# Performance work log

Measured on AMD Instinct MI355X. Metric: run time of the kernel, lower is better.

## Reference

```python
import jax, jax.numpy as jnp
import numpy as np

N_FEAT = 32
P = 3            # patch_size
K = 4            # top-k
DS = (3, 5, 7)   # displacement windows for (l3, l2, l1)
T = 3            # n_frames
EPS = 1e-12      # F.normalize eps


def _unfold(x, ksz):
    # F.unfold(x, ksz, padding=ksz//2, stride=1): [b,c,h,w] -> [b,c,ksz*ksz,h,w]
    b, c, h, w = x.shape
    pad = ksz // 2
    xp = jnp.pad(x, ((0, 0), (0, 0), (pad, pad), (pad, pad)))
    pats = [xp[:, :, i:i + h, j:j + w] for i in range(ksz) for j in range(ksz)]
    return jnp.stack(pats, axis=2)


def _agg_unit(feat_t, feat_tm1, d, agg_w, agg_b, wp_w, wp_b):
    b, c, h, w = feat_t.shape
    p2 = P * P
    ft_u = _unfold(feat_t, P).reshape(b, c * p2, h, w)        # [b,cp2,h,w]
    ftm_u = _unfold(feat_tm1, P).reshape(b, c * p2, h, w)     # [b,cp2,h,w]
    disp = jnp.transpose(_unfold(ftm_u, d), (0, 1, 3, 4, 2))  # [b,cp2,h,w,d2]
    # cosine similarity over channel*patch dim
    ft_n = ft_u / jnp.maximum(jnp.linalg.norm(ft_u, axis=1, keepdims=True), EPS)
    disp_norm = jnp.maximum(jnp.linalg.norm(disp, axis=1), EPS)          # [b,h,w,d2]
    sim = jnp.einsum('bchw,bchwd->bhwd', ft_n, disp) / disp_norm          # [b,h,w,d2]
    _, idx = jax.lax.top_k(sim, K)                                        # [b,h,w,K]
    gath = jnp.take_along_axis(disp, idx[:, None], axis=-1)               # [b,cp2,h,w,K]
    g = gath.reshape(b, c, p2, h, w, K)
    # aggregator: Conv2d(K,1,1) == weighted sum over K + scalar bias
    aggd = jnp.einsum('bcphwk,k->bcphw', g, agg_w) + agg_b                # [b,c,p2,h,w]
    aggd = jnp.transpose(aggd, (0, 1, 3, 4, 2))                           # [b,c,h,w,p2]
    # w_proj: Conv2d(2c, c*p2, 1)
    wm = jnp.einsum('oi,bihw->bohw', wp_w, jnp.concatenate([feat_t, feat_tm1], axis=1))
    wm = wm + wp_b[None, :, None, None]
    wm = jnp.transpose(wm.reshape(b, c, p2, h, w), (0, 1, 3, 4, 2))       # [b,c,h,w,p2]
    return jnp.sum(aggd * wm, axis=-1)                                    # [b,c,h,w]


def _up2(x):
    # bilinear x2, align_corners=False (half-pixel == jax.image 'linear')
    b, c, h, w = x.shape
    return jax.image.resize(x, (b, c, 2 * h, 2 * w), method='linear')


def _pixel_shuffle(x, r):
    b, c, h, w = x.shape
    co = c // (r * r)
    x = x.reshape(b, co, r, r, h, w)
    return jnp.transpose(x, (0, 1, 4, 2, 5, 3)).reshape(b, co, h * r, w * r)


def setup_inputs() -> dict:
    key = jax.random.key(0)
    ks = jax.random.split(key, 20)
    B, C, H = 1, N_FEAT, 48
    p2 = P * P
    d = {}
    d['feats_l1'] = jax.random.normal(ks[0], (B, C, T, H, H), jnp.float32)
    d['feats_l2'] = jax.random.normal(ks[1], (B, C, T, H // 2, H // 2), jnp.float32)
    d['feats_l3'] = jax.random.normal(ks[2], (B, C, T, H // 4, H // 4), jnp.float32)
    for i, name in enumerate(['l3', 'l2', 'l1']):
        d['agg_' + name + '_w'] = jax.random.normal(ks[3 + 4 * i], (K,), jnp.float32) * 0.1
        d['agg_' + name + '_b'] = jax.random.normal(ks[4 + 4 * i], (), jnp.float32) * 0.1
        d['wp_' + name + '_w'] = jax.random.normal(ks[5 + 4 * i], (C * p2, 2 * C), jnp.float32) * 0.05
        d['wp_' + name + '_b'] = jnp.zeros((C * p2,), jnp.float32)
    d['up_w'] = jax.random.normal(ks[16], (4 * C, C * T), jnp.float32) * 0.05
    d['up_b'] = jnp.zeros((4 * C,), jnp.float32)
    return d


def reference(feats_l1, feats_l2, feats_l3,
              agg_l3_w, agg_l3_b, wp_l3_w, wp_l3_b,
              agg_l2_w, agg_l2_b, wp_l2_w, wp_l2_b,
              agg_l1_w, agg_l1_b, wp_l1_w, wp_l1_b,
              up_w, up_b):
    center = T // 2
    c1 = feats_l1[:, :, center]
    c2 = feats_l2[:, :, center]
    c3 = feats_l3[:, :, center]
    a3 = [_up2(_agg_unit(c3, feats_l3[:, :, t], DS[0], agg_l3_w, agg_l3_b, wp_l3_w, wp_l3_b))
          for t in range(T)]
    a2 = [_up2(_agg_unit(c2 + a3[t], feats_l2[:, :, t] + a3[t], DS[1], agg_l2_w, agg_l2_b, wp_l2_w, wp_l2_b))
          for t in range(T)]
    a1 = [_agg_unit(c1 + a2[t], feats_l1[:, :, t] + a2[t], DS[2], agg_l1_w, agg_l1_b, wp_l1_w, wp_l1_b)
          for t in range(T)]
    x = jnp.concatenate(a1, axis=1)                                       # [b, c*T, h, w]
    x = jnp.einsum('oi,bihw->bohw', up_w, x) + up_b[None, :, None, None]  # [b, 4c, h, w]
    return _pixel_shuffle(x, 2)                                           # [b, c, 2h, 2w]
```

## Files before the change

### kernel.cpp

```cpp
#include <hip/hip_runtime.h>
#include <math.h>


template<int D, int TS, int H, int W, bool HA>
__global__ __launch_bounds__(256, 4)
void agg_tile(const float* __restrict__ feats,
              const float* __restrict__ add,
              const float* __restrict__ agg_w,
              const float* __restrict__ agg_b,
              const float* __restrict__ wp_w,
              const float* __restrict__ wp_b,
              float* __restrict__ out)
{
    constexpr int PD = D / 2;
    constexpr int M  = PD + 1;
    constexpr int R  = TS + 2 * M;
    constexpr int S  = TS + 2;
    constexpr int S2 = S * S;
    constexpr int D2 = D * D;
    constexpr int NP = TS * TS;
    constexpr int NX = S2 * D2;
    constexpr int NSIM = NP * D2;
    constexpr int CS = 36;
    constexpr int USZ = (NP * 288 > NX + NSIM) ? NP * 288 : NX + NSIM;
    constexpr int TPW = W / TS;
    constexpr int NPA = R * R;
    constexpr int GA  = 256 / NPA;
    constexpr int NPS = S * S;
    constexpr int GS  = 256 / NPS;

    __shared__ float sA[NPA * CS];
    __shared__ float sC[NPS * CS];
    __shared__ float t2[NPA];
    __shared__ float s2[NPS];
    __shared__ float U[USZ];
    __shared__ int   sIdx[NP * 4];

    float* Xarr = U;
    float* sSim = U + NX;

    const int tid  = threadIdx.x;
    const int tile = blockIdx.x;
    const int t    = blockIdx.y;
    const int y0 = (tile / TPW) * TS;
    const int x0 = (tile % TPW) * TS;

    const float* addT = HA ? (add + (size_t)t * 32 * H * W) : nullptr;

    if (tid < NPA * GA) {
        const int pos = tid % NPA;
        const int cb  = tid / NPA;
        const int ry = pos / R, rx = pos % R;
        const int yy = y0 - M + ry, xx = x0 - M + rx;
        float* dst = sA + pos * CS;
        if (yy >= 0 && yy < H && xx >= 0 && xx < W) {
            const float* sF = feats + (((size_t)cb * 3 + t) * H + yy) * W + xx;
            const float* sD = HA ? (addT + ((size_t)cb * H + yy) * W + xx) : nullptr;
            #pragma unroll 1
            for (int c = cb; c < 32; c += GA) {
                float v = *sF; sF += GA * 3 * H * W;
                if (HA) { v += *sD; sD += GA * H * W; }
                dst[c] = v;
            }
        } else {
            #pragma unroll 1
            for (int c = cb; c < 32; c += GA) dst[c] = 0.f;
        }
    }
    if (tid < NPS * GS) {
        const int pos = tid % NPS;
        const int cb  = tid / NPS;
        const int ry = pos / S, rx = pos % S;
        const int yy = y0 - 1 + ry, xx = x0 - 1 + rx;
        float* dst = sC + pos * CS;
        if (yy >= 0 && yy < H && xx >= 0 && xx < W) {
            const float* sF = feats + (((size_t)cb * 3 + 1) * H + yy) * W + xx;
            const float* sD = HA ? (addT + ((size_t)cb * H + yy) * W + xx) : nullptr;
            #pragma unroll 1
            for (int c = cb; c < 32; c += GS) {
                float v = *sF; sF += GS * 3 * H * W;
                if (HA) { v += *sD; sD += GS * H * W; }
                dst[c] = v;
            }
        } else {
            #pragma unroll 1
            for (int c = cb; c < 32; c += GS) dst[c] = 0.f;
        }
    }
    __syncthreads();

    if (tid < S2 * D) {
        const int u  = tid / D;
        const int di = tid - u * D;
        const int uy = u / S, ux = u - uy * S;
        float4 cv[8];
        const float4* c4 = (const float4*)(sC + u * CS);
        #pragma unroll
        for (int i = 0; i < 8; ++i) cv[i] = c4[i];
        const float* arow = sA + ((uy + di) * R + ux) * CS;
        float* xrow = Xarr + u * D2 + di * D;
        #pragma unroll
        for (int dj = 0; dj < D; ++dj) {
            const float4* a4 = (const float4*)(arow + dj * CS);
            float s = 0.f;
            #pragma unroll
            for (int i = 0; i < 8; ++i) {
                float4 av = a4[i];
                s += cv[i].x * av.x + cv[i].y * av.y + cv[i].z * av.z + cv[i].w * av.w;
            }
            xrow[dj] = s;
        }
    }
    for (int e = tid; e < NPA; e += 256) {
        const float4* a4 = (const float4*)(sA + e * CS);
        float s = 0.f;
        #pragma unroll
        for (int cc = 0; cc < 8; ++cc) {
            float4 v = a4[cc];
            s += v.x * v.x + v.y * v.y + v.z * v.z + v.w * v.w;
        }
        t2[e] = s;
    }
    for (int e = tid; e < NPS; e += 256) {
        const float4* c4 = (const float4*)(sC + e * CS);
        float s = 0.f;
        #pragma unroll
        for (int cc = 0; cc < 8; ++cc) {
            float4 v = c4[cc];
            s += v.x * v.x + v.y * v.y + v.z * v.z + v.w * v.w;
        }
        s2[e] = s;
    }
    __syncthreads();

    for (int e = tid; e < NSIM; e += 256) {
        int p = e / D2, dd = e - p * D2;
        int py = p / TS, px = p - py * TS;
        int di = dd / D, dj = dd - di * D;
        int Yc = y0 + py + di - PD, Xc = x0 + px + dj - PD;
        float sim = 0.f;
        if (Yc >= 0 && Yc < H && Xc >= 0 && Xc < W) {
            float dot = 0.f, n2 = 0.f, nf = 0.f;
            #pragma unroll
            for (int qi = 0; qi < 3; ++qi)
            #pragma unroll
            for (int qj = 0; qj < 3; ++qj) {
                dot += Xarr[((py + qi) * S + (px + qj)) * D2 + dd];
                n2  += t2[(py + qi + di) * R + (px + qj + dj)];
                nf  += s2[(py + qi) * S + (px + qj)];
            }
            sim = dot / fmaxf(sqrtf(nf), 1e-12f) / fmaxf(sqrtf(n2), 1e-12f);
        }
        sSim[e] = sim;
    }
    __syncthreads();

    if (tid < NP) {
        float v0 = -3.0e38f, v1 = -3.0e38f, v2 = -3.0e38f, v3 = -3.0e38f;
        int   i0 = 0, i1 = 0, i2 = 0, i3 = 0;
        const float* row = sSim + tid * D2;
        for (int dd = 0; dd < D2; ++dd) {
            float v = row[dd];
            if (v > v0)      { v3=v2;i3=i2; v2=v1;i2=i1; v1=v0;i1=i0; v0=v;i0=dd; }
            else if (v > v1) { v3=v2;i3=i2; v2=v1;i2=i1; v1=v;i1=dd; }
            else if (v > v2) { v3=v2;i3=i2; v2=v;i2=dd; }
            else if (v > v3) { v3=v;i3=dd; }
        }
        int py = tid / TS, px = tid - (tid / TS) * TS;
        int ids[4] = {i0, i1, i2, i3};
        #pragma unroll
        for (int k = 0; k < 4; ++k) {
            int dd = ids[k];
            int di = dd / D, dj = dd - di * D;
            int Yc = y0 + py + di - PD, Xc = x0 + px + dj - PD;
            sIdx[tid * 4 + k] = (Yc >= 0 && Yc < H && Xc >= 0 && Xc < W)
                              ? (di * R + dj) * CS : -1;
        }
    }
    __syncthreads();

    const float4* wp4 = (const float4*)wp_w;
    for (int o = tid; o < 288; o += 256) {
        float4 w[8];
        #pragma unroll
        for (int i = 0; i < 8; ++i) w[i] = wp4[o * 16 + i];
        const float wb = wp_b[o];
        int py = 0, px = 0;
        #pragma unroll 1
        for (int p = 0; p < NP; ++p) {
            const float4* pv4 = (const float4*)(sC + ((py + 1) * S + (px + 1)) * CS);
            float acc = wb;
            #pragma unroll
            for (int i = 0; i < 8; ++i) {
                float4 pv = pv4[i];
                acc += w[i].x * pv.x + w[i].y * pv.y + w[i].z * pv.z + w[i].w * pv.w;
            }
            U[p * 288 + o] = acc;
            if (++px == TS) { px = 0; ++py; }
        }
    }
    const float aw0 = agg_w[0], aw1 = agg_w[1], aw2 = agg_w[2], aw3 = agg_w[3];
    const float ab  = agg_b[0];
    for (int o = tid; o < 288; o += 256) {
        const int c = o / 9, q = o - (o / 9) * 9;
        const int qi = q / 3, qj = q - (q / 3) * 3;
        const int qoff = (qi * R + qj) * CS + c;
        float4 w[8];
        #pragma unroll
        for (int i = 0; i < 8; ++i) w[i] = wp4[o * 16 + 8 + i];
        int py = 0, px = 0;
        #pragma unroll 1
        for (int p = 0; p < NP; ++p) {
            const float4* pv4 = (const float4*)(sA + ((py + M) * R + (px + M)) * CS);
            float acc = U[p * 288 + o];
            #pragma unroll
            for (int i = 0; i < 8; ++i) {
                float4 pv = pv4[i];
                acc += w[i].x * pv.x + w[i].y * pv.y + w[i].z * pv.z + w[i].w * pv.w;
            }
            const int gbase = (py * R + px) * CS + qoff;
            float aggd = ab;
            #pragma unroll
            for (int k = 0; k < 4; ++k) {
                int soff = sIdx[p * 4 + k];
                if (soff >= 0) {
                    float val = sA[gbase + soff];
                    float aw = (k == 0) ? aw0 : (k == 1) ? aw1 : (k == 2) ? aw2 : aw3;
                    aggd += aw * val;
                }
            }
            U[p * 288 + o] = aggd * acc;
            if (++px == TS) { px = 0; ++py; }
        }
    }
    __syncthreads();

    for (int e = tid; e < 32 * NP; e += 256) {
        int c = e / NP, p = e - (e / NP) * NP;
        int py = p / TS, px = p - (p / TS) * TS;
        float s = 0.f;
        const float* up = U + p * 288 + c * 9;
        #pragma unroll
        for (int q = 0; q < 9; ++q) s += up[q];
        out[((t * 32 + c) * H + (y0 + py)) * W + (x0 + px)] = s;
    }
}

__global__ void up2_kernel(const float* __restrict__ in, float* __restrict__ out,
                           int C, int h, int w)
{
    int idx = blockIdx.x * blockDim.x + threadIdx.x;
    int H = 2 * h, W = 2 * w;
    int total = C * H * W;
    if (idx >= total) return;
    int ox = idx % W;
    int oy = (idx / W) % H;
    int c  = idx / (W * H);

    int my = oy >> 1, mx = ox >> 1;
    int y0, y1, x0, x1;
    float wy0, wy1, wx0, wx1;
    if ((oy & 1) == 0) { y0 = max(my - 1, 0); y1 = my; wy0 = 0.25f; wy1 = 0.75f; }
    else               { y0 = my; y1 = min(my + 1, h - 1); wy0 = 0.75f; wy1 = 0.25f; }
    if ((ox & 1) == 0) { x0 = max(mx - 1, 0); x1 = mx; wx0 = 0.25f; wx1 = 0.75f; }
    else               { x0 = mx; x1 = min(mx + 1, w - 1); wx0 = 0.75f; wx1 = 0.25f; }

    const float* pc = in + (size_t)c * h * w;
    float v = wy0 * (wx0 * pc[y0 * w + x0] + wx1 * pc[y0 * w + x1])
            + wy1 * (wx0 * pc[y1 * w + x0] + wx1 * pc[y1 * w + x1]);
    out[idx] = v;
}

__global__ __launch_bounds__(256)
void final_kernel(const float* __restrict__ a1,
                  const float* __restrict__ up_w,
                  const float* __restrict__ up_b,
                  float* __restrict__ out)
{
    const int pix = blockIdx.x * 256 + threadIdx.x;
    const int o   = blockIdx.y;
    const int x = pix % 48, y = pix / 48;

    const float* w = up_w + o * 96;
    float acc = up_b[o];
    #pragma unroll 4
    for (int i = 0; i < 96; ++i) acc += w[i] * a1[i * 2304 + pix];

    int co = o >> 2, ry = (o >> 1) & 1, rx = o & 1;
    out[((co * 96 + 2 * y + ry) * 96) + 2 * x + rx] = acc;
}

extern "C" void kernel_launch(void* const* d_in, const int* in_sizes, int n_in,
                              void* d_out, int out_size, void* d_ws, size_t ws_size,
                              hipStream_t stream)
{
    const float* feats_l1 = (const float*)d_in[0];
    const float* feats_l2 = (const float*)d_in[1];
    const float* feats_l3 = (const float*)d_in[2];
    const float* agg_l3_w = (const float*)d_in[3];
    const float* agg_l3_b = (const float*)d_in[4];
    const float* wp_l3_w  = (const float*)d_in[5];
    const float* wp_l3_b  = (const float*)d_in[6];
    const float* agg_l2_w = (const float*)d_in[7];
    const float* agg_l2_b = (const float*)d_in[8];
    const float* wp_l2_w  = (const float*)d_in[9];
    const float* wp_l2_b  = (const float*)d_in[10];
    const float* agg_l1_w = (const float*)d_in[11];
    const float* agg_l1_b = (const float*)d_in[12];
    const float* wp_l1_w  = (const float*)d_in[13];
    const float* wp_l1_b  = (const float*)d_in[14];
    const float* up_w     = (const float*)d_in[15];
    const float* up_b     = (const float*)d_in[16];
    float* out = (float*)d_out;

    float* ws   = (float*)d_ws;
    float* agg3 = ws;
    float* a3up = agg3 + 13824;
    float* agg2 = a3up + 55296;
    float* a2up = agg2 + 55296;
    float* a1   = a2up + 221184;

    agg_tile<3, 1, 12, 12, false><<<dim3(144, 3), 256, 0, stream>>>(
        feats_l3, nullptr, agg_l3_w, agg_l3_b, wp_l3_w, wp_l3_b, agg3);
    up2_kernel<<<(96 * 24 * 24 + 255) / 256, 256, 0, stream>>>(agg3, a3up, 96, 12, 12);

    agg_tile<5, 2, 24, 24, true><<<dim3(144, 3), 256, 0, stream>>>(
        feats_l2, a3up, agg_l2_w, agg_l2_b, wp_l2_w, wp_l2_b, agg2);
    up2_kernel<<<(96 * 48 * 48 + 255) / 256, 256, 0, stream>>>(agg2, a2up, 96, 24, 24);

    agg_tile<7, 3, 48, 48, true><<<dim3(256, 3), 256, 0, stream>>>(
        feats_l1, a2up, agg_l1_w, agg_l1_b, wp_l1_w, wp_l1_b, a1);

    final_kernel<<<dim3(9, 128), 256, 0, stream>>>(a1, up_w, up_b, out);
}
```

Baseline: 161.2 us.

## Fuse all pipeline stages into one cooperative persistent kernel with grid syncs

Replaces six separate kernel launches (three aggregation stages, two upsamples, and the final projection) with a single cooperative kernel of 768 blocks. The stages are separated by grid-wide syncs, and shared memory is carved manually from one static buffer. This removes per-launch overhead and inter-kernel gaps. In exchange it adds grid barrier costs, forces one shared-memory and register footprint across every stage, and requires all 768 blocks to be co-resident.

```diff
diff --git a/kernel.cpp b/kernel.cpp
--- a/kernel.cpp
+++ b/kernel.cpp
@@ -1,16 +1,20 @@
 #include <hip/hip_runtime.h>
+#include <hip/hip_cooperative_groups.h>
 #include <math.h>
 
+namespace cg = cooperative_groups;
+
 
 template<int D, int TS, int H, int W, bool HA>
-__global__ __launch_bounds__(256, 4)
-void agg_tile(const float* __restrict__ feats,
-              const float* __restrict__ add,
-              const float* __restrict__ agg_w,
-              const float* __restrict__ agg_b,
-              const float* __restrict__ wp_w,
-              const float* __restrict__ wp_b,
-              float* __restrict__ out)
+__device__ void agg_dev(float* __restrict__ smemF,
+                        const float* __restrict__ feats,
+                        const float* __restrict__ add,
+                        const float* __restrict__ agg_w,
+                        const float* __restrict__ agg_b,
+                        const float* __restrict__ wp_w,
+                        const float* __restrict__ wp_b,
+                        float* __restrict__ out,
+                        const int tile, const int t)
 {
     constexpr int PD = D / 2;
     constexpr int M  = PD + 1;
@@ -29,19 +33,17 @@
     constexpr int NPS = S * S;
     constexpr int GS  = 256 / NPS;
 
-    __shared__ float sA[NPA * CS];
-    __shared__ float sC[NPS * CS];
-    __shared__ float t2[NPA];
-    __shared__ float s2[NPS];
-    __shared__ float U[USZ];
-    __shared__ int   sIdx[NP * 4];
+    float* sA = smemF;
+    float* sC = sA + NPA * CS;
+    float* t2 = sC + NPS * CS;
+    float* s2 = t2 + NPA;
+    float* U  = s2 + NPS;
+    int* sIdx = (int*)(U + USZ);
 
     float* Xarr = U;
     float* sSim = U + NX;
 
-    const int tid  = threadIdx.x;
-    const int tile = blockIdx.x;
-    const int t    = blockIdx.y;
+    const int tid = threadIdx.x;
     const int y0 = (tile / TPW) * TS;
     const int x0 = (tile % TPW) * TS;
 
@@ -244,15 +246,14 @@
         for (int q = 0; q < 9; ++q) s += up[q];
         out[((t * 32 + c) * H + (y0 + py)) * W + (x0 + px)] = s;
     }
+    __syncthreads();
 }
 
-__global__ void up2_kernel(const float* __restrict__ in, float* __restrict__ out,
-                           int C, int h, int w)
+__device__ __forceinline__ void up2_elem(const float* __restrict__ in,
+                                         float* __restrict__ out,
+                                         int h, int w, int idx)
 {
-    int idx = blockIdx.x * blockDim.x + threadIdx.x;
-    int H = 2 * h, W = 2 * w;
-    int total = C * H * W;
-    if (idx >= total) return;
+    const int W = 2 * w, H = 2 * h;
     int ox = idx % W;
     int oy = (idx / W) % H;
     int c  = idx / (W * H);
@@ -266,53 +267,68 @@
     else               { x0 = mx; x1 = min(mx + 1, w - 1); wx0 = 0.75f; wx1 = 0.25f; }
 
     const float* pc = in + (size_t)c * h * w;
-    float v = wy0 * (wx0 * pc[y0 * w + x0] + wx1 * pc[y0 * w + x1])
-            + wy1 * (wx0 * pc[y1 * w + x0] + wx1 * pc[y1 * w + x1]);
-    out[idx] = v;
+    out[idx] = wy0 * (wx0 * pc[y0 * w + x0] + wx1 * pc[y0 * w + x1])
+             + wy1 * (wx0 * pc[y1 * w + x0] + wx1 * pc[y1 * w + x1]);
 }
 
-__global__ __launch_bounds__(256)
-void final_kernel(const float* __restrict__ a1,
-                  const float* __restrict__ up_w,
-                  const float* __restrict__ up_b,
-                  float* __restrict__ out)
+struct MegaParams {
+    const float *f1, *f2, *f3;
+    const float *aw3, *ab3, *wpw3, *wpb3;
+    const float *aw2, *ab2, *wpw2, *wpb2;
+    const float *aw1, *ab1, *wpw1, *wpb1;
+    const float *upw, *upb;
+    float *agg3, *a3up, *agg2, *a2up, *a1, *out;
+};
+
+__global__ __launch_bounds__(256, 4)
+void mega(MegaParams p)
 {
-    const int pix = blockIdx.x * 256 + threadIdx.x;
-    const int o   = blockIdx.y;
-    const int x = pix % 48, y = pix / 48;
-
-    const float* w = up_w + o * 96;
-    float acc = up_b[o];
-    #pragma unroll 4
-    for (int i = 0; i < 96; ++i) acc += w[i] * a1[i * 2304 + pix];
-
-    int co = o >> 2, ry = (o >> 1) & 1, rx = o & 1;
-    out[((co * 96 + 2 * y + ry) * 96) + 2 * x + rx] = acc;
+    __shared__ __align__(16) float smem[8064];
+    cg::grid_group grid = cg::this_grid();
+    const int b = blockIdx.x;
+    const int tid = threadIdx.x;
+
+    if (b < 432)
+        agg_dev<3, 1, 12, 12, false>(smem, p.f3, nullptr, p.aw3, p.ab3,
+                                     p.wpw3, p.wpb3, p.agg3, b % 144, b / 144);
+    grid.sync();
+
+    {
+        int idx = b * 256 + tid;
+        if (idx < 96 * 24 * 24) up2_elem(p.agg3, p.a3up, 12, 12, idx);
+    }
+    grid.sync();
+
+    if (b < 432)
+        agg_dev<5, 2, 24, 24, true>(smem, p.f2, p.a3up, p.aw2, p.ab2,
+                                    p.wpw2, p.wpb2, p.agg2, b % 144, b / 144);
+    grid.sync();
+
+    for (int idx = b * 256 + tid; idx < 96 * 48 * 48; idx += 768 * 256)
+        up2_elem(p.agg2, p.a2up, 24, 24, idx);
+    grid.sync();
+
+    agg_dev<7, 3, 48, 48, true>(smem, p.f1, p.a2up, p.aw1, p.ab1,
+                                p.wpw1, p.wpb1, p.a1, b % 256, b / 256);
+    grid.sync();
+
+    for (int bu = b; bu < 1152; bu += 768) {
+        const int o   = bu / 9;
+        const int pix = (bu - o * 9) * 256 + tid;
+        const int x = pix % 48, y = pix / 48;
+        const float* w = p.upw + o * 96;
+        float acc = p.upb[o];
+        #pragma unroll 4
+        for (int i = 0; i < 96; ++i) acc += w[i] * p.a1[i * 2304 + pix];
+        int co = o >> 2, ry = (o >> 1) & 1, rx = o & 1;
+        p.out[((co * 96 + 2 * y + ry) * 96) + 2 * x + rx] = acc;
+    }
 }
 
 extern "C" void kernel_launch(void* const* d_in, const int* in_sizes, int n_in,
                               void* d_out, int out_size, void* d_ws, size_t ws_size,
                               hipStream_t stream)
 {
-    const float* feats_l1 = (const float*)d_in[0];
-    const float* feats_l2 = (const float*)d_in[1];
-    const float* feats_l3 = (const float*)d_in[2];
-    const float* agg_l3_w = (const float*)d_in[3];
-    const float* agg_l3_b = (const float*)d_in[4];
-    const float* wp_l3_w  = (const float*)d_in[5];
-    const float* wp_l3_b  = (const float*)d_in[6];
-    const float* agg_l2_w = (const float*)d_in[7];
-    const float* agg_l2_b = (const float*)d_in[8];
-    const float* wp_l2_w  = (const float*)d_in[9];
-    const float* wp_l2_b  = (const float*)d_in[10];
-    const float* agg_l1_w = (const float*)d_in[11];
-    const float* agg_l1_b = (const float*)d_in[12];
-    const float* wp_l1_w  = (const float*)d_in[13];
-    const float* wp_l1_b  = (const float*)d_in[14];
-    const float* up_w     = (const float*)d_in[15];
-    const float* up_b     = (const float*)d_in[16];
-    float* out = (float*)d_out;
-
     float* ws   = (float*)d_ws;
     float* agg3 = ws;
     float* a3up = agg3 + 13824;
@@ -320,16 +336,27 @@
     float* a2up = agg2 + 55296;
     float* a1   = a2up + 221184;
 
-    agg_tile<3, 1, 12, 12, false><<<dim3(144, 3), 256, 0, stream>>>(
-        feats_l3, nullptr, agg_l3_w, agg_l3_b, wp_l3_w, wp_l3_b, agg3);
-    up2_kernel<<<(96 * 24 * 24 + 255) / 256, 256, 0, stream>>>(agg3, a3up, 96, 12, 12);
-
-    agg_tile<5, 2, 24, 24, true><<<dim3(144, 3), 256, 0, stream>>>(
-        feats_l2, a3up, agg_l2_w, agg_l2_b, wp_l2_w, wp_l2_b, agg2);
-    up2_kernel<<<(96 * 48 * 48 + 255) / 256, 256, 0, stream>>>(agg2, a2up, 96, 24, 24);
-
-    agg_tile<7, 3, 48, 48, true><<<dim3(256, 3), 256, 0, stream>>>(
-        feats_l1, a2up, agg_l1_w, agg_l1_b, wp_l1_w, wp_l1_b, a1);
-
-    final_kernel<<<dim3(9, 128), 256, 0, stream>>>(a1, up_w, up_b, out);
+    MegaParams mp;
+    mp.f1   = (const float*)d_in[0];
+    mp.f2   = (const float*)d_in[1];
+    mp.f3   = (const float*)d_in[2];
+    mp.aw3  = (const float*)d_in[3];
+    mp.ab3  = (const float*)d_in[4];
+    mp.wpw3 = (const float*)d_in[5];
+    mp.wpb3 = (const float*)d_in[6];
+    mp.aw2  = (const float*)d_in[7];
+    mp.ab2  = (const float*)d_in[8];
+    mp.wpw2 = (const float*)d_in[9];
+    mp.wpb2 = (const float*)d_in[10];
+    mp.aw1  = (const float*)d_in[11];
+    mp.ab1  = (const float*)d_in[12];
+    mp.wpw1 = (const float*)d_in[13];
+    mp.wpb1 = (const float*)d_in[14];
+    mp.upw  = (const float*)d_in[15];
+    mp.upb  = (const float*)d_in[16];
+    mp.agg3 = agg3; mp.a3up = a3up; mp.agg2 = agg2; mp.a2up = a2up; mp.a1 = a1;
+    mp.out  = (float*)d_out;
+
+    void* args[] = { &mp };
+    hipLaunchCooperativeKernel(mega, dim3(768), dim3(256), args, 0, stream);
 }
```

Result: slower. 584.3 us (+262.4%).
